# Performance work log

Measured on AMD Instinct MI355X. Metric: run time of the kernel, lower is better.

Reference implementation:

```python
import jax, jax.numpy as jnp
import numpy as np

D_MODEL = 1024
N_HEADS = 16
D_K = D_MODEL // N_HEADS
T_MIN = 0.01
T_MAX = 2.0
B = 4
S = 1024


def setup_inputs() -> dict:
    key = jax.random.key(0)
    ks = jax.random.split(key, 16)
    sc = 1.0 / np.sqrt(D_MODEL).astype(np.float32)
    inp = {
        'query': jax.random.normal(ks[0], (B, S, D_MODEL), jnp.float32),
        'key': jax.random.normal(ks[1], (B, S, D_MODEL), jnp.float32),
        'value': jax.random.normal(ks[2], (B, S, D_MODEL), jnp.float32),
        # Linear weights stored as (in, out); torch does x @ W.T + b with W (out,in)
        'Wq': jax.random.normal(ks[3], (D_MODEL, D_MODEL), jnp.float32) * sc,
        'bq': jax.random.normal(ks[4], (D_MODEL,), jnp.float32) * 0.01,
        'Wk': jax.random.normal(ks[5], (D_MODEL, D_MODEL), jnp.float32) * sc,
        'bk': jax.random.normal(ks[6], (D_MODEL,), jnp.float32) * 0.01,
        'Wv': jax.random.normal(ks[7], (D_MODEL, D_MODEL), jnp.float32) * sc,
        'bv': jax.random.normal(ks[8], (D_MODEL,), jnp.float32) * 0.01,
        'Wo': jax.random.normal(ks[9], (D_MODEL, D_MODEL), jnp.float32) * sc,
        'bo': jax.random.normal(ks[10], (D_MODEL,), jnp.float32) * 0.01,
        # time-predictor MLP: Linear(3,16) -> tanh -> Linear(16,1)
        'Wt1': jax.random.normal(ks[11], (3, 16), jnp.float32) * 0.5,
        'bt1': jax.random.normal(ks[12], (16,), jnp.float32) * 0.1,
        'Wt2': jax.random.normal(ks[13], (16, 1), jnp.float32) * 0.25,
        'bt2': jax.random.normal(ks[14], (1,), jnp.float32) * 0.1,
    }
    return inp


def _forward(query, key, value, Wq, bq, Wk, bk, Wv, bv, Wo, bo, Wt1, bt1, Wt2, bt2):
    Bq, Sq, D = query.shape
    Sk = key.shape[1]

    def proj(x, W, b, Slen):
        return (x @ W + b).reshape(Bq, Slen, N_HEADS, D_K).transpose(0, 2, 1, 3)

    Q = proj(query, Wq, bq, Sq)   # (B,H,Sq,dk)
    K = proj(key, Wk, bk, Sk)     # (B,H,Sk,dk)
    V = proj(value, Wv, bv, Sk)   # (B,H,Sk,dk)

    # --- DiffusionTimePredictor (fp32) ---
    Qf = Q.astype(jnp.float32)
    Kf = K.astype(jnp.float32)
    inv_sqrt_dk = np.float32(1.0 / np.sqrt(D_K))
    s = jnp.einsum('bhqd,bhkd->bhqk', Qf, Kf) * inv_sqrt_dk
    s = jnp.clip(s, -50.0, 50.0)
    mean_sim = s.mean(axis=(-2, -1))                       # (B,H)
    max_sim = s.max(axis=-1).mean(axis=-1)                 # (B,H)
    probs = jax.nn.softmax(s / 2.0, axis=-1)
    entropy_proxy = probs.var(axis=-1, ddof=1).mean(axis=-1)  # torch var unbiased=True
    mean_sim = jnp.clip(jnp.nan_to_num(mean_sim), -10.0, 10.0)
    max_sim = jnp.clip(jnp.nan_to_num(max_sim), -10.0, 10.0)
    entropy_proxy = jnp.clip(jnp.nan_to_num(entropy_proxy, nan=0.1), 0.0, 1.0)
    feats = jnp.stack([mean_sim, max_sim, entropy_proxy], axis=-1)  # (B,H,3)
    raw_t = jnp.tanh(feats @ Wt1 + bt1) @ Wt2 + bt2                  # (B,H,1)
    t = T_MIN + jax.nn.sigmoid(raw_t) * (T_MAX - T_MIN)
    t = jnp.clip(t, T_MIN, T_MAX)[..., None].astype(query.dtype)     # (B,H,1,1)
    t = jnp.minimum(t, 0.85)                                          # clamp(max=0.85)

    # --- heat kernel attention ---
    scores = jnp.einsum('bhqd,bhkd->bhqk', Q, K) / (2.0 * t)
    attn = jnp.nan_to_num(jax.nn.softmax(scores, axis=-1))
    out = jnp.einsum('bhqk,bhkd->bhqd', attn, V)
    out = out.transpose(0, 2, 1, 3).reshape(Bq, Sq, D)
    return out @ Wo + bo


def reference(query, key, value, Wq, bq, Wk, bk, Wv, bv, Wo, bo, Wt1, bt1, Wt2, bt2):
    return _forward(query, key, value, Wq, bq, Wk, bk, Wv, bv, Wo, bo, Wt1, bt1, Wt2, bt2)
```

## Files before the change

### kernel.cpp

```cpp
#include <hip/hip_runtime.h>
#include <hip/hip_bf16.h>
#include <math.h>

#define SS   1024
#define DM   1024
#define NH   16
#define DKH  64
#define NB   4
#define NBH  64

typedef unsigned short ush;
typedef unsigned int uint32;
typedef __attribute__((ext_vector_type(8))) short bf8_t;
typedef __attribute__((ext_vector_type(4))) float f32x4;
#define MFMA16(a,b,c) __builtin_amdgcn_mfma_f32_16x16x32_bf16((a),(b),(c),0,0,0)

__device__ __forceinline__ ush f2bf(float x){ return __bfloat16_as_ushort(__float2bfloat16(x)); }
__device__ __forceinline__ uint32 pk2(float a, float b){
  return (uint32)f2bf(a) | ((uint32)f2bf(b) << 16);
}
__device__ __forceinline__ int swz8(int row, int chunk){
  return row*64 + (((chunk) ^ (row & 7)) << 3);
}

__global__ __launch_bounds__(256) void xconv(
    const float* __restrict__ q, const float* __restrict__ k, const float* __restrict__ v,
    ush* __restrict__ xq, ush* __restrict__ xk, ush* __restrict__ xv)
{
  const float* src = (blockIdx.y==0)?q:(blockIdx.y==1)?k:v;
  ush* dst = (blockIdx.y==0)?xq:(blockIdx.y==1)?xk:xv;
  const size_t i = ((size_t)blockIdx.x*256 + threadIdx.x)*8;
  float4 a = *(const float4*)&src[i];
  float4 b = *(const float4*)&src[i+4];
  uint4 o;
  o.x = pk2(a.x, a.y); o.y = pk2(a.z, a.w);
  o.z = pk2(b.x, b.y); o.w = pk2(b.z, b.w);
  *(uint4*)&dst[i] = o;
}

__global__ void wconv4(const float* __restrict__ W0, const float* __restrict__ W1,
                       const float* __restrict__ W2, const float* __restrict__ W3,
                       ush* __restrict__ H0, ush* __restrict__ H1,
                       ush* __restrict__ H2, ush* __restrict__ H3)
{
  __shared__ float T[32][33];
  const int tx = threadIdx.x, ty = threadIdx.y;
  const int z = blockIdx.z;
  const float* W = (z==0)?W0:(z==1)?W1:(z==2)?W2:W3;
  ush* H = (z==0)?H0:(z==1)?H1:(z==2)?H2:H3;
  const int k0 = blockIdx.y*32, n0 = blockIdx.x*32;
  #pragma unroll
  for (int i = 0; i < 4; ++i){
    int r = ty + 8*i;
    T[r][tx] = W[(size_t)(k0 + r)*DM + n0 + tx];
  }
  __syncthreads();
  #pragma unroll
  for (int i = 0; i < 4; ++i){
    int r = ty + 8*i;
    H[(size_t)(n0 + r)*DM + k0 + tx] = f2bf(T[tx][r]);
  }
}

__global__ __launch_bounds__(256) void proj_qkv(
    const ush* __restrict__ xq, const ush* __restrict__ xk, const ush* __restrict__ xv,
    const ush* __restrict__ Wqh, const ush* __restrict__ Wkh, const ush* __restrict__ Wvh,
    const float* __restrict__ bq, const float* __restrict__ bk,
    const float* __restrict__ bv,
    ush* __restrict__ Qb, ush* __restrict__ Kb, ush* __restrict__ Vt)
{
  __shared__ ush SMEM[16896];

  const int fid = blockIdx.x;
  const int glob = (fid & 7)*96 + (fid >> 3);
  const int z = glob >> 8, rem = glob & 255;
  const int m0 = (rem >> 3) * 128, n0 = (rem & 7) * 128;

  const ush* A  = (z==0) ? xq  : (z==1) ? xk  : xv;
  const ush* Bh = (z==0) ? Wqh : (z==1) ? Wkh : Wvh;

  const int tid = threadIdx.x;
  const int lane = tid & 63, w = tid >> 6;
  const int c = lane & 15, g = lane >> 4;
  const int wr = w >> 1, wc = w & 1;

  f32x4 acc[4][4];
  #pragma unroll
  for (int i = 0; i < 4; ++i)
    #pragma unroll
    for (int j = 0; j < 4; ++j) acc[i][j] = (f32x4){0.f,0.f,0.f,0.f};

  const int prow0 = w*16 + (lane >> 3), prow1 = prow0 + 8;
  const int jj = lane & 7;
  const int sg0 = jj ^ (prow0 & 7), sg1 = jj ^ (prow1 & 7);
  const size_t aoff0 = (size_t)(2*prow0 + (sg0 >> 2))*DM + (sg0 & 3)*8;
  const size_t aoff1 = (size_t)(2*prow1 + (sg1 >> 2))*DM + (sg1 & 3)*8;
  const ush* Aab = A  + (size_t)m0*DM;
  const ush* Bhb = Bh + (size_t)n0*DM;
  const int lb0 = w*1024, lb1 = w*1024 + 512;

#define GLL(GP, LIDX) __builtin_amdgcn_global_load_lds( \
    (const __attribute__((address_space(1))) unsigned int*)(GP), \
    (__attribute__((address_space(3))) unsigned int*)(&SMEM[LIDX]), 16, 0, 0)

#define ISSUE_PROJ(BUFO, KT) do{ \
    GLL(Aab + aoff0 + (KT), (BUFO) + lb0); \
    GLL(Aab + aoff1 + (KT), (BUFO) + lb1); \
    GLL(Bhb + aoff0 + (KT), (BUFO) + 4096 + lb0); \
    GLL(Bhb + aoff1 + (KT), (BUFO) + 4096 + lb1); \
  }while(0)

  const int csw = (((4*(c & 1) + g) ^ ((c >> 1) & 7)) << 3);

  ISSUE_PROJ(0, 0);
  int cur = 0;
  for (int kt = 0; kt < DM; kt += 32){
    __syncthreads();
    if (kt + 32 < DM) ISSUE_PROJ((cur ^ 1)*8192, kt + 32);

    const ush* As  = SMEM + cur*8192;
    const ush* Bhs = As + 4096;

    bf8_t a_h[4];
    #pragma unroll
    for (int fm = 0; fm < 4; ++fm)
      a_h[fm] = *(const bf8_t*)&As[(32*wr + 8*fm + (c>>1))*64 + csw];
    __builtin_amdgcn_s_setprio(1);
    #pragma unroll
    for (int fn = 0; fn < 4; ++fn){
      bf8_t b_h = *(const bf8_t*)&Bhs[(32*wc + 8*fn + (c>>1))*64 + csw];
      #pragma unroll
      for (int fm = 0; fm < 4; ++fm)
        acc[fm][fn] = MFMA16(a_h[fm], b_h, acc[fm][fn]);
    }
    __builtin_amdgcn_s_setprio(0);
    cur ^= 1;
  }
#undef ISSUE_PROJ
#undef GLL

  if (z < 2){
    ush* O = (z==0) ? Qb : Kb;
    const float* bias = (z==0) ? bq : bk;
    #pragma unroll
    for (int fm = 0; fm < 4; ++fm){
      #pragma unroll
      for (int fn = 0; fn < 4; ++fn){
        const int col = n0 + 64*wc + 16*fn + c;
        const float bb = bias[col];
        const int row0 = m0 + 64*wr + 16*fm + 4*g;
        const int hd = col >> 6, d = col & 63;
        #pragma unroll
        for (int r = 0; r < 4; ++r){
          const int row = row0 + r;
          const int b = row >> 10, s = row & 1023;
          O[((size_t)(b*NH + hd)*SS + s)*DKH + d] = f2bf(acc[fm][fn][r] + bb);
        }
      }
    }
  } else {
    __syncthreads();
    ush* Vep = SMEM + w*4224;
    #pragma unroll
    for (int fm = 0; fm < 4; ++fm){
      #pragma unroll
      for (int fn = 0; fn < 4; ++fn){
        const float bb = bv[n0 + 64*wc + 16*fn + c];
        #pragma unroll
        for (int r = 0; r < 4; ++r)
          Vep[(16*fn + c)*66 + 16*fm + 4*g + r] = f2bf(acc[fm][fn][r] + bb);
      }
    }
    const int b = m0 >> 10;
    const int s0 = (m0 & 1023) + 64*wr;
    const int hd = (n0 >> 6) + wc;
    const size_t vbase = ((size_t)(b*NH + hd))*DKH*SS;
    #pragma unroll
    for (int it = 0; it < 8; ++it){
      const int dr = 8*it + (lane >> 3);
      const int sc = (lane & 7)*8;
      uint4 vv = *(const uint4*)&Vep[dr*66 + sc];
      *(uint4*)&Vt[vbase + (size_t)dr*SS + s0 + sc] = vv;
    }
  }
}

__global__ __launch_bounds__(256) void gemm_out(
    const ush* __restrict__ Abf, const ush* __restrict__ Bth,
    const float* __restrict__ bias, float* __restrict__ outf)
{
  __shared__ ush As[4096], Bs[2048];

  const int fid = blockIdx.x;
  const int glob = (fid & 7)*64 + (fid >> 3);
  const int m0 = (glob >> 4)*128, n0 = (glob & 15)*64;

  const int tid = threadIdx.x;
  const int lane = tid & 63, w = tid >> 6;
  const int c = lane & 15, g = lane >> 4;
  const int wr = w >> 1, wc = w & 1;

  f32x4 acc[4][2];
  #pragma unroll
  for (int i = 0; i < 4; ++i){ acc[i][0] = (f32x4){0,0,0,0}; acc[i][1] = (f32x4){0,0,0,0}; }

  const int prow = tid >> 3, ci = tid & 7;
  const int lr   = 2*prow + (ci >> 2);
  const int koff = (ci & 3) << 3;
  const int ws0  = prow*64 + ((ci ^ (prow & 7)) << 3);
  const int ws1  = ws0 + 32*64;
  const int csw  = (((4*(c & 1) + g) ^ ((c >> 1) & 7)) << 3);

  uint4 ar0, ar1, brr;
  #define ISSUE_OUT(KT) do{ \
    ar0 = *(const uint4*)(Abf + (size_t)(m0 + lr)*DM + (KT) + koff); \
    ar1 = *(const uint4*)(Abf + (size_t)(m0 + lr + 64)*DM + (KT) + koff); \
    brr = *(const uint4*)(Bth + (size_t)(n0 + lr)*DM + (KT) + koff); \
  }while(0)

  ISSUE_OUT(0);
  for (int kt = 0; kt < DM; kt += 32){
    *(uint4*)&As[ws0] = ar0;
    *(uint4*)&As[ws1] = ar1;
    if (lr < 64) *(uint4*)&Bs[ws0] = brr;
    __syncthreads();
    if (kt + 32 < DM) ISSUE_OUT(kt + 32);

    bf8_t a_h[4];
    #pragma unroll
    for (int fm = 0; fm < 4; ++fm)
      a_h[fm] = *(const bf8_t*)&As[(32*wr + 8*fm + (c>>1))*64 + csw];
    #pragma unroll
    for (int fn = 0; fn < 2; ++fn){
      bf8_t b_h = *(const bf8_t*)&Bs[(16*wc + 8*fn + (c>>1))*64 + csw];
      #pragma unroll
      for (int fm = 0; fm < 4; ++fm)
        acc[fm][fn] = MFMA16(a_h[fm], b_h, acc[fm][fn]);
    }
    __syncthreads();
  }
  #undef ISSUE_OUT

  #pragma unroll
  for (int fm = 0; fm < 4; ++fm){
    #pragma unroll
    for (int fn = 0; fn < 2; ++fn){
      const int col = n0 + 32*wc + 16*fn + c;
      const float bb = bias[col];
      const int row0 = m0 + 64*wr + 16*fm + 4*g;
      #pragma unroll
      for (int r = 0; r < 4; ++r)
        outf[(size_t)(row0 + r)*DM + col] = acc[fm][fn][r] + bb;
    }
  }
}

__global__ __launch_bounds__(512) void attn_stats_mfma(
    const ush* __restrict__ Qb, const ush* __restrict__ Kb,
    float* __restrict__ stats)
{
  __shared__ ush Khs[64*64];
  __shared__ float red[8][3];
  const int tid = threadIdx.x, lane = tid & 63, w = tid >> 6;
  const int c = lane & 15, g = lane >> 4;
  const int fid = blockIdx.x;
  const int glob = (fid & 7)*64 + (fid >> 3);
  const int bh = glob >> 3, q0 = (glob & 7)*128;

  bf8_t qh[2];
  {
    const ush* qp = Qb + ((size_t)bh*SS + q0 + 16*w + c)*DKH + 8*g;
    qh[0] = *(const bf8_t*)(qp);
    qh[1] = *(const bf8_t*)(qp + 32);
  }

  float ssum = 0.f, rmax = -1e30f, lsum = 0.f, l2sum = 0.f;
  const int rr0 = tid >> 3, ci = tid & 7;

  uint4 k0;
  #define ISSUE_ST(KC) do{ \
    k0 = *(const uint4*)(Kb + ((size_t)bh*SS + (KC)*64 + rr0)*DKH + ci*8); \
  }while(0)

  ISSUE_ST(0);
  for (int kc = 0; kc < 16; ++kc){
    *(uint4*)&Khs[swz8(rr0, ci)] = k0;
    __syncthreads();
    if (kc < 15) ISSUE_ST(kc + 1);

    f32x4 sa[4];
    #pragma unroll
    for (int fn = 0; fn < 4; ++fn) sa[fn] = (f32x4){0.f,0.f,0.f,0.f};
    __builtin_amdgcn_s_setprio(1);
    #pragma unroll
    for (int fn = 0; fn < 4; ++fn){
      #pragma unroll
      for (int ds = 0; ds < 2; ++ds){
        bf8_t ah = *(const bf8_t*)&Khs[swz8(16*fn + c, g + 4*ds)];
        sa[fn] = MFMA16(ah, qh[ds], sa[fn]);
      }
    }
    __builtin_amdgcn_s_setprio(0);
    #pragma unroll
    for (int fn = 0; fn < 4; ++fn){
      #pragma unroll
      for (int r = 0; r < 4; ++r){
        float s = sa[fn][r] * 0.125f;
        ssum += s;
        rmax = fmaxf(rmax, s);
        float e = exp2f(s * 0.7213475204f);
        lsum += e;
        l2sum = fmaf(e, e, l2sum);
      }
    }
    __syncthreads();
  }
  #undef ISSUE_ST

  rmax  = fmaxf(rmax, __shfl_xor(rmax, 16, 64));
  rmax  = fmaxf(rmax, __shfl_xor(rmax, 32, 64));
  lsum  += __shfl_xor(lsum, 16, 64);   lsum  += __shfl_xor(lsum, 32, 64);
  l2sum += __shfl_xor(l2sum, 16, 64);  l2sum += __shfl_xor(l2sum, 32, 64);
  float varc = (l2sum/(lsum*lsum) - (1.0f/1024.f)) * (1.0f/1023.f);
  float a0 = ssum, a1 = rmax * 0.25f, a2 = varc * 0.25f;
  #pragma unroll
  for (int off = 1; off < 64; off <<= 1){
    a0 += __shfl_xor(a0, off, 64);
    a1 += __shfl_xor(a1, off, 64);
    a2 += __shfl_xor(a2, off, 64);
  }
  if (lane == 0){ red[w][0] = a0; red[w][1] = a1; red[w][2] = a2; }
  __syncthreads();
  if (tid == 0){
    float r0 = 0.f, r1 = 0.f, r2 = 0.f;
    #pragma unroll
    for (int i = 0; i < 8; ++i){ r0 += red[i][0]; r1 += red[i][1]; r2 += red[i][2]; }
    atomicAdd(&stats[bh*4+0], r0);
    atomicAdd(&stats[bh*4+1], r1);
    atomicAdd(&stats[bh*4+2], r2);
  }
}

__global__ __launch_bounds__(512) void attn_flash_mfma(
    const ush* __restrict__ Qb, const ush* __restrict__ Kb,
    const ush* __restrict__ Vt, const float* __restrict__ stats,
    const float* __restrict__ Wt1, const float* __restrict__ bt1,
    const float* __restrict__ Wt2, const float* __restrict__ bt2,
    ush* __restrict__ aout)
{
  __shared__ ush Khs[64*64], Vts[64*64], Ps[128*64];
  __shared__ float tshare;
  const int tid = threadIdx.x, lane = tid & 63, w = tid >> 6;
  const int c = lane & 15, g = lane >> 4;
  const int fid = blockIdx.x;
  const int glob = (fid & 7)*64 + (fid >> 3);
  const int bh = glob >> 3, q0 = (glob & 7)*128;

  if (tid < 16){
    float mean = fminf(fmaxf(stats[bh*4+0] * (1.f/(1024.f*1024.f)), -10.f), 10.f);
    float mx   = fminf(fmaxf(stats[bh*4+1] * (1.f/1024.f), -10.f), 10.f);
    float ent  = fminf(fmaxf(stats[bh*4+2] * (1.f/1024.f),   0.f),  1.f);
    float h = tanhf(mean*Wt1[tid] + mx*Wt1[16+tid] + ent*Wt1[32+tid] + bt1[tid])
              * Wt2[tid];
    h += __shfl_xor(h, 1, 64);
    h += __shfl_xor(h, 2, 64);
    h += __shfl_xor(h, 4, 64);
    h += __shfl_xor(h, 8, 64);
    if (tid == 0){
      float raw = h + bt2[0];
      float sig = 1.f / (1.f + expf(-raw));
      float t = 0.01f + sig * 1.99f;
      t = fminf(fminf(fmaxf(t, 0.01f), 2.0f), 0.85f);
      tshare = (0.5f / t) * 1.44269504f;
    }
  }

  bf8_t qh[2];
  {
    const ush* qp = Qb + ((size_t)bh*SS + q0 + 16*w + c)*DKH + 8*g;
    qh[0] = *(const bf8_t*)(qp);
    qh[1] = *(const bf8_t*)(qp + 32);
  }

  f32x4 o[4];
  #pragma unroll
  for (int i = 0; i < 4; ++i) o[i] = (f32x4){0.f,0.f,0.f,0.f};
  float m = -INFINITY, lpart = 0.f;

  const int rr0 = tid >> 3, ci = tid & 7;

  uint4 k0, vr0;
  #define ISSUE_FL(KC) do{ \
    k0  = *(const uint4*)(Kb + ((size_t)bh*SS + (KC)*64 + rr0)*DKH + ci*8); \
    vr0 = *(const uint4*)(Vt + ((size_t)bh*DKH + rr0)*SS + (KC)*64 + ci*8); \
  }while(0)

  ISSUE_FL(0);
  *(uint4*)&Khs[swz8(rr0, ci)] = k0;
  *(uint4*)&Vts[swz8(rr0, ci)] = vr0;
  __syncthreads();
  const float tsc2 = tshare;

  for (int kc = 0; kc < 16; ++kc){
    if (kc){
      *(uint4*)&Khs[swz8(rr0, ci)] = k0;
      *(uint4*)&Vts[swz8(rr0, ci)] = vr0;
      __syncthreads();
    }
    if (kc < 15) ISSUE_FL(kc + 1);

    f32x4 sa[4];
    #pragma unroll
    for (int fn = 0; fn < 4; ++fn) sa[fn] = (f32x4){0.f,0.f,0.f,0.f};
    __builtin_amdgcn_s_setprio(1);
    #pragma unroll
    for (int fn = 0; fn < 4; ++fn){
      #pragma unroll
      for (int ds = 0; ds < 2; ++ds){
        bf8_t ah = *(const bf8_t*)&Khs[swz8(16*fn + c, g + 4*ds)];
        sa[fn] = MFMA16(ah, qh[ds], sa[fn]);
      }
    }
    __builtin_amdgcn_s_setprio(0);

    float pmaxr = -1e30f;
    #pragma unroll
    for (int fn = 0; fn < 4; ++fn)
      #pragma unroll
      for (int r = 0; r < 4; ++r) pmaxr = fmaxf(pmaxr, sa[fn][r]);

    if (!__all(pmaxr * tsc2 <= m + 30.f)){
      pmaxr = fmaxf(pmaxr, __shfl_xor(pmaxr, 16, 64));
      pmaxr = fmaxf(pmaxr, __shfl_xor(pmaxr, 32, 64));
      float pmax = pmaxr * tsc2;
      float mn = fmaxf(m, pmax);
      float sc = exp2f(m - mn);
      m = mn;
      lpart *= sc;
      #pragma unroll
      for (int r = 0; r < 4; ++r){
        float so = __shfl(sc, 4*g + r, 16);
        #pragma unroll
        for (int fn = 0; fn < 4; ++fn) o[fn][r] *= so;
      }
    }

    const float mneg = -m;
    #pragma unroll
    for (int fn = 0; fn < 4; ++fn){
      float e0 = exp2f(fmaf(sa[fn][0], tsc2, mneg));
      float e1 = exp2f(fmaf(sa[fn][1], tsc2, mneg));
      float e2 = exp2f(fmaf(sa[fn][2], tsc2, mneg));
      float e3 = exp2f(fmaf(sa[fn][3], tsc2, mneg));
      lpart += (e0 + e1) + (e2 + e3);
      uint2 pk;
      pk.x = pk2(e0, e1);
      pk.y = pk2(e2, e3);
      const int q4 = 4*fn + g;
      const int addr = (16*w + c)*64 + ((((q4 >> 1) ^ (c & 7)) << 3)) + (q4 & 1)*4;
      *(uint2*)&Ps[addr] = pk;
    }

    __builtin_amdgcn_s_setprio(1);
    #pragma unroll
    for (int kvs = 0; kvs < 2; ++kvs){
      bf8_t pa = *(const bf8_t*)&Ps[swz8(16*w + c, g + 4*kvs)];
      #pragma unroll
      for (int fn = 0; fn < 4; ++fn){
        bf8_t vb = *(const bf8_t*)&Vts[swz8(16*fn + c, g + 4*kvs)];
        o[fn] = MFMA16(pa, vb, o[fn]);
      }
    }
    __builtin_amdgcn_s_setprio(0);
    __syncthreads();
  }
  #undef ISSUE_FL

  lpart += __shfl_xor(lpart, 16, 64);
  lpart += __shfl_xor(lpart, 32, 64);
  const int b = bh >> 4, hd = bh & 15;
  #pragma unroll
  for (int r = 0; r < 4; ++r){
    float linv = 1.f / __shfl(lpart, 4*g + r, 16);
    const int q = q0 + 16*w + 4*g + r;
    #pragma unroll
    for (int fn = 0; fn < 4; ++fn)
      aout[((size_t)(b*SS + q))*DM + hd*DKH + 16*fn + c] = f2bf(o[fn][r] * linv);
  }
}

extern "C" void kernel_launch(void* const* d_in, const int* in_sizes, int n_in,
                              void* d_out, int out_size, void* d_ws, size_t ws_size,
                              hipStream_t stream)
{
  const float* query = (const float*)d_in[0];
  const float* key   = (const float*)d_in[1];
  const float* value = (const float*)d_in[2];
  const float* Wq = (const float*)d_in[3];
  const float* bq = (const float*)d_in[4];
  const float* Wk = (const float*)d_in[5];
  const float* bk = (const float*)d_in[6];
  const float* Wv = (const float*)d_in[7];
  const float* bv = (const float*)d_in[8];
  const float* Wo = (const float*)d_in[9];
  const float* bo = (const float*)d_in[10];
  const float* Wt1 = (const float*)d_in[11];
  const float* bt1 = (const float*)d_in[12];
  const float* Wt2 = (const float*)d_in[13];
  const float* bt2 = (const float*)d_in[14];

  const size_t E = (size_t)NB*SS*DM;
  const size_t WE = (size_t)DM*DM;

  ush* Qbb = (ush*)d_ws;
  ush* Kbb = Qbb + E;
  ush* Vtb = Kbb + E;
  ush* Aob = Vtb + E;
  ush* xqb = Aob;
  ush* xkb = Aob + E;
  ush* xvb = xkb + E;
  ush* Wqh = xvb + E;
  ush* Wkh = Wqh + WE;
  ush* Wvh = Wkh + WE;
  ush* Woh = Wvh + WE;
  float* stats = (float*)(Woh + WE);

  hipMemsetAsync(stats, 0, 4*NBH*sizeof(float), stream);

  xconv<<<dim3(2048, 3), 256, 0, stream>>>(query, key, value, xqb, xkb, xvb);

  dim3 wb(32, 8), wg(32, 32, 4);
  wconv4<<<wg, wb, 0, stream>>>(Wq, Wk, Wv, Wo, Wqh, Wkh, Wvh, Woh);

  proj_qkv<<<768, 256, 0, stream>>>(xqb, xkb, xvb,
      Wqh, Wkh, Wvh, bq, bk, bv, Qbb, Kbb, Vtb);

  attn_stats_mfma<<<512, 512, 0, stream>>>(Qbb, Kbb, stats);
  attn_flash_mfma<<<512, 512, 0, stream>>>(Qbb, Kbb, Vtb, stats,
      Wt1, bt1, Wt2, bt2, Aob);

  gemm_out<<<512, 256, 0, stream>>>(Aob, Woh, bo, (float*)d_out);
}
```

Measured before the change: 144.6 us.

## Fuse fp32-to-bf16 input conversion into QKV projection GEMM

Removes the separate xconv kernel that converted query/key/value from fp32 to bf16. The projection GEMM now streams fp32 activation tiles into LDS with async global-to-LDS loads using a new swizzle and converts them to bf16 in registers before the MFMAs. This saves one launch and a full bf16 write plus re-read of three activation tensors. In exchange the GEMM reads twice the bytes for A, uses more LDS per block (possibly lowering occupancy), and does conversion work on every tile, repeated across the N-tile blocks.

```diff
diff --git a/kernel.cpp b/kernel.cpp
--- a/kernel.cpp
+++ b/kernel.cpp
@@ -22,21 +22,7 @@
 __device__ __forceinline__ int swz8(int row, int chunk){
   return row*64 + (((chunk) ^ (row & 7)) << 3);
 }
-
-__global__ __launch_bounds__(256) void xconv(
-    const float* __restrict__ q, const float* __restrict__ k, const float* __restrict__ v,
-    ush* __restrict__ xq, ush* __restrict__ xk, ush* __restrict__ xv)
-{
-  const float* src = (blockIdx.y==0)?q:(blockIdx.y==1)?k:v;
-  ush* dst = (blockIdx.y==0)?xq:(blockIdx.y==1)?xk:xv;
-  const size_t i = ((size_t)blockIdx.x*256 + threadIdx.x)*8;
-  float4 a = *(const float4*)&src[i];
-  float4 b = *(const float4*)&src[i+4];
-  uint4 o;
-  o.x = pk2(a.x, a.y); o.y = pk2(a.z, a.w);
-  o.z = pk2(b.x, b.y); o.w = pk2(b.z, b.w);
-  *(uint4*)&dst[i] = o;
-}
+union U4B8 { uint4 u; bf8_t b; };
 
 __global__ void wconv4(const float* __restrict__ W0, const float* __restrict__ W1,
                        const float* __restrict__ W2, const float* __restrict__ W3,
@@ -63,21 +49,22 @@
 }
 
 __global__ __launch_bounds__(256) void proj_qkv(
-    const ush* __restrict__ xq, const ush* __restrict__ xk, const ush* __restrict__ xv,
+    const float* __restrict__ xq, const float* __restrict__ xk, const float* __restrict__ xv,
     const ush* __restrict__ Wqh, const ush* __restrict__ Wkh, const ush* __restrict__ Wvh,
     const float* __restrict__ bq, const float* __restrict__ bk,
     const float* __restrict__ bv,
     ush* __restrict__ Qb, ush* __restrict__ Kb, ush* __restrict__ Vt)
 {
-  __shared__ ush SMEM[16896];
+  __shared__ ush SMEM[24576];
+  float* SMEMf = (float*)SMEM;
 
   const int fid = blockIdx.x;
   const int glob = (fid & 7)*96 + (fid >> 3);
   const int z = glob >> 8, rem = glob & 255;
   const int m0 = (rem >> 3) * 128, n0 = (rem & 7) * 128;
 
-  const ush* A  = (z==0) ? xq  : (z==1) ? xk  : xv;
-  const ush* Bh = (z==0) ? Wqh : (z==1) ? Wkh : Wvh;
+  const float* A = (z==0) ? xq  : (z==1) ? xk  : xv;
+  const ush* Bh  = (z==0) ? Wqh : (z==1) ? Wkh : Wvh;
 
   const int tid = threadIdx.x;
   const int lane = tid & 63, w = tid >> 6;
@@ -90,41 +77,59 @@
     #pragma unroll
     for (int j = 0; j < 4; ++j) acc[i][j] = (f32x4){0.f,0.f,0.f,0.f};
 
+  const int arowg = lane >> 3;
+  const int asw   = ((lane & 7) ^ arowg) << 2;
+  const float* Aab = A + (size_t)m0*DM;
+
   const int prow0 = w*16 + (lane >> 3), prow1 = prow0 + 8;
   const int jj = lane & 7;
   const int sg0 = jj ^ (prow0 & 7), sg1 = jj ^ (prow1 & 7);
-  const size_t aoff0 = (size_t)(2*prow0 + (sg0 >> 2))*DM + (sg0 & 3)*8;
-  const size_t aoff1 = (size_t)(2*prow1 + (sg1 >> 2))*DM + (sg1 & 3)*8;
-  const ush* Aab = A  + (size_t)m0*DM;
+  const size_t boff0 = (size_t)(2*prow0 + (sg0 >> 2))*DM + (sg0 & 3)*8;
+  const size_t boff1 = (size_t)(2*prow1 + (sg1 >> 2))*DM + (sg1 & 3)*8;
   const ush* Bhb = Bh + (size_t)n0*DM;
   const int lb0 = w*1024, lb1 = w*1024 + 512;
 
-#define GLL(GP, LIDX) __builtin_amdgcn_global_load_lds( \
+#define GLLF(GP, FIDX) __builtin_amdgcn_global_load_lds( \
     (const __attribute__((address_space(1))) unsigned int*)(GP), \
-    (__attribute__((address_space(3))) unsigned int*)(&SMEM[LIDX]), 16, 0, 0)
-
-#define ISSUE_PROJ(BUFO, KT) do{ \
-    GLL(Aab + aoff0 + (KT), (BUFO) + lb0); \
-    GLL(Aab + aoff1 + (KT), (BUFO) + lb1); \
-    GLL(Bhb + aoff0 + (KT), (BUFO) + 4096 + lb0); \
-    GLL(Bhb + aoff1 + (KT), (BUFO) + 4096 + lb1); \
+    (__attribute__((address_space(3))) unsigned int*)(&SMEMf[FIDX]), 16, 0, 0)
+#define GLLU(GP, UIDX) __builtin_amdgcn_global_load_lds( \
+    (const __attribute__((address_space(1))) unsigned int*)(GP), \
+    (__attribute__((address_space(3))) unsigned int*)(&SMEM[UIDX]), 16, 0, 0)
+
+#define ISSUE_PROJ(BUFO_F, BUFO_U, KT) do{ \
+    GLLF(Aab + (size_t)(w*32 + 0*8 + arowg)*DM + asw + (KT), (BUFO_F) + w*1024 + 0*256); \
+    GLLF(Aab + (size_t)(w*32 + 1*8 + arowg)*DM + asw + (KT), (BUFO_F) + w*1024 + 1*256); \
+    GLLF(Aab + (size_t)(w*32 + 2*8 + arowg)*DM + asw + (KT), (BUFO_F) + w*1024 + 2*256); \
+    GLLF(Aab + (size_t)(w*32 + 3*8 + arowg)*DM + asw + (KT), (BUFO_F) + w*1024 + 3*256); \
+    GLLU(Bhb + boff0 + (KT), (BUFO_U) + lb0); \
+    GLLU(Bhb + boff1 + (KT), (BUFO_U) + lb1); \
   }while(0)
 
   const int csw = (((4*(c & 1) + g) ^ ((c >> 1) & 7)) << 3);
-
-  ISSUE_PROJ(0, 0);
+  const int cs0 = ((2*g)     ^ (c & 7)) << 2;
+  const int cs1 = ((2*g + 1) ^ (c & 7)) << 2;
+
+  ISSUE_PROJ(0, 8192, 0);
   int cur = 0;
   for (int kt = 0; kt < DM; kt += 32){
     __syncthreads();
-    if (kt + 32 < DM) ISSUE_PROJ((cur ^ 1)*8192, kt + 32);
-
-    const ush* As  = SMEM + cur*8192;
-    const ush* Bhs = As + 4096;
+    if (kt + 32 < DM) ISSUE_PROJ((cur ^ 1)*6144, (cur ^ 1)*12288 + 8192, kt + 32);
+
+    const float* Afp = SMEMf + cur*6144;
+    const ush*   Bhs = SMEM + cur*12288 + 8192;
 
     bf8_t a_h[4];
     #pragma unroll
-    for (int fm = 0; fm < 4; ++fm)
-      a_h[fm] = *(const bf8_t*)&As[(32*wr + 8*fm + (c>>1))*64 + csw];
+    for (int fm = 0; fm < 4; ++fm){
+      const int arow = 64*wr + 16*fm + c;
+      float av[8];
+      *(float4*)&av[0] = *(const float4*)&Afp[arow*32 + cs0];
+      *(float4*)&av[4] = *(const float4*)&Afp[arow*32 + cs1];
+      U4B8 t;
+      t.u = (uint4){pk2(av[0],av[1]), pk2(av[2],av[3]),
+                    pk2(av[4],av[5]), pk2(av[6],av[7])};
+      a_h[fm] = t.b;
+    }
     __builtin_amdgcn_s_setprio(1);
     #pragma unroll
     for (int fn = 0; fn < 4; ++fn){
@@ -137,7 +142,8 @@
     cur ^= 1;
   }
 #undef ISSUE_PROJ
-#undef GLL
+#undef GLLF
+#undef GLLU
 
   if (z < 2){
     ush* O = (z==0) ? Qb : Kb;
@@ -516,10 +522,7 @@
   ush* Kbb = Qbb + E;
   ush* Vtb = Kbb + E;
   ush* Aob = Vtb + E;
-  ush* xqb = Aob;
-  ush* xkb = Aob + E;
-  ush* xvb = xkb + E;
-  ush* Wqh = xvb + E;
+  ush* Wqh = Aob + E;
   ush* Wkh = Wqh + WE;
   ush* Wvh = Wkh + WE;
   ush* Woh = Wvh + WE;
@@ -527,12 +530,10 @@
 
   hipMemsetAsync(stats, 0, 4*NBH*sizeof(float), stream);
 
-  xconv<<<dim3(2048, 3), 256, 0, stream>>>(query, key, value, xqb, xkb, xvb);
-
   dim3 wb(32, 8), wg(32, 32, 4);
   wconv4<<<wg, wb, 0, stream>>>(Wq, Wk, Wv, Wo, Wqh, Wkh, Wvh, Woh);
 
-  proj_qkv<<<768, 256, 0, stream>>>(xqb, xkb, xvb,
+  proj_qkv<<<768, 256, 0, stream>>>(query, key, value,
       Wqh, Wkh, Wvh, bq, bk, bv, Qbb, Kbb, Vtb);
 
   attn_stats_mfma<<<512, 512, 0, stream>>>(Qbb, Kbb, stats);
```

After: 161.2 us. 1.12x slower.
